# Optimization experiments

Hardware: AMD Instinct MI355X
Metric: run time of the kernel (lower is better)

## Reference

```python
import jax, jax.numpy as jnp
from jax import lax
import numpy as np

R = 4            # correlation displacement radius -> 81 channels
BACKWARP = 1.25  # fltBackwarp for intLevel=4


def leaky(x):
    return jnp.where(x >= 0, x, 0.1 * x)


def conv2d(x, w, b):
    # 3x3, stride 1, pad 1, NCHW/OIHW
    y = lax.conv_general_dilated(x, w, (1, 1), ((1, 1), (1, 1)),
                                 dimension_numbers=('NCHW', 'OIHW', 'NCHW'))
    return y + b[None, :, None, None]


def conv_transpose2d(x, w, b):
    # PyTorch ConvTranspose2d(k=4, s=2, p=1); w is (Cin, Cout, 4, 4)
    wt = jnp.transpose(jnp.flip(w, (2, 3)), (1, 0, 2, 3))  # -> OIHW
    y = lax.conv_general_dilated(x, wt, (1, 1), ((2, 2), (2, 2)),
                                 lhs_dilation=(2, 2),
                                 dimension_numbers=('NCHW', 'OIHW', 'NCHW'))
    return y + b[None, :, None, None]


def correlation(f1, f2):
    # cost volume: mean over channels of f1 * shifted f2, zero padding, 81 taps
    B, C, H, W = f1.shape
    f2p = jnp.pad(f2, ((0, 0), (0, 0), (R, R), (R, R)))
    outs = [jnp.mean(f1 * lax.dynamic_slice(f2p, (0, 0, dy, dx), (B, C, H, W)), axis=1)
            for dy in range(2 * R + 1) for dx in range(2 * R + 1)]
    return jnp.stack(outs, axis=1)  # (B, 81, H, W)


def flow_warp(feat, flow):
    # bilinear grid_sample, padding_mode='zeros', align_corners=True
    # align_corners=True normalization round-trips, so sample at pixel coords
    B, C, H, W = feat.shape
    ys, xs = jnp.meshgrid(jnp.arange(H, dtype=flow.dtype),
                          jnp.arange(W, dtype=flow.dtype), indexing='ij')
    px = xs[None] + flow[:, 0]  # (B,H,W)
    py = ys[None] + flow[:, 1]
    x0 = jnp.floor(px); y0 = jnp.floor(py)
    wx = px - x0; wy = py - y0
    featl = jnp.transpose(feat, (0, 2, 3, 1))  # (B,H,W,C)
    bidx = jnp.arange(B)[:, None, None]

    def gather(yi, xi):
        valid = (yi >= 0) & (yi < H) & (xi >= 0) & (xi < W)
        yc = jnp.clip(yi, 0, H - 1).astype(jnp.int32)
        xc = jnp.clip(xi, 0, W - 1).astype(jnp.int32)
        return featl[bidx, yc, xc] * valid[..., None].astype(feat.dtype)

    out = (gather(y0, x0) * ((1 - wy) * (1 - wx))[..., None]
           + gather(y0, x0 + 1) * ((1 - wy) * wx)[..., None]
           + gather(y0 + 1, x0) * (wy * (1 - wx))[..., None]
           + gather(y0 + 1, x0 + 1) * (wy * wx)[..., None])
    return jnp.transpose(out, (0, 3, 1, 2))


def setup_inputs() -> dict:
    key = jax.random.key(0)
    ks = jax.random.split(key, 24)
    B, C, H, W = 8, 96, 64, 128
    intCurrent = 81 + 96 + 2 + 2          # 181
    prevC = (81 + 128 + 2 + 2) + 128 + 128 + 96 + 64 + 32  # 661
    s = 0.05
    inp = {
        'tenOne': jax.random.normal(ks[0], (B, C, H, W), jnp.float32),
        'tenTwo': jax.random.normal(ks[1], (B, C, H, W), jnp.float32),
        'prev_flow': jax.random.normal(ks[2], (B, 2, H // 2, W // 2), jnp.float32),
        'prev_feat': jax.random.normal(ks[3], (B, prevC, H // 2, W // 2), jnp.float32),
        'w_upflow': jax.random.normal(ks[4], (2, 2, 4, 4), jnp.float32) * s,
        'b_upflow': jax.random.normal(ks[5], (2,), jnp.float32) * s,
        'w_upfeat': jax.random.normal(ks[6], (prevC, 2, 4, 4), jnp.float32) * s,
        'b_upfeat': jax.random.normal(ks[7], (2,), jnp.float32) * s,
    }
    c = intCurrent
    dims = [(128, c), (128, c + 128), (96, c + 256), (64, c + 352), (32, c + 416), (2, c + 448)]
    for i, (co, ci) in enumerate(dims):
        inp[f'w{i+1}'] = jax.random.normal(ks[8 + 2 * i], (co, ci, 3, 3), jnp.float32) * s
        inp[f'b{i+1}'] = jax.random.normal(ks[9 + 2 * i], (co,), jnp.float32) * s
    return inp


def reference(tenOne, tenTwo, prev_flow, prev_feat,
              w_upflow, b_upflow, w_upfeat, b_upfeat,
              w1, b1, w2, b2, w3, b3, w4, b4, w5, b5, w6, b6):
    tenFlow = conv_transpose2d(prev_flow, w_upflow, b_upflow)   # (B,2,H,W)
    upFeat = conv_transpose2d(prev_feat, w_upfeat, b_upfeat)    # (B,2,H,W)
    warped = flow_warp(tenTwo, tenFlow * BACKWARP)
    vol = leaky(correlation(tenOne, warped))                    # (B,81,H,W)
    feat = jnp.concatenate([vol, tenOne, tenFlow, upFeat], axis=1)  # 181 ch
    feat = jnp.concatenate([leaky(conv2d(feat, w1, b1)), feat], axis=1)
    feat = jnp.concatenate([leaky(conv2d(feat, w2, b2)), feat], axis=1)
    feat = jnp.concatenate([leaky(conv2d(feat, w3, b3)), feat], axis=1)
    feat = jnp.concatenate([leaky(conv2d(feat, w4, b4)), feat], axis=1)
    feat = jnp.concatenate([leaky(conv2d(feat, w5, b5)), feat], axis=1)
    flow = leaky(conv2d(feat, w6, b6))                          # netSix is a ConvBlock
    return flow, feat
```

## Files before the change

kernel.cpp:

```cpp
#include <hip/hip_runtime.h>

#define W 128
#define H 64
#define HW 8192
#define NB 8
#define NPIX 65536
#define CHSZ 2097152L

typedef __attribute__((ext_vector_type(8))) short short8;
typedef __attribute__((ext_vector_type(4))) float floatx4;

__device__ __forceinline__ float leakyf(float v) { return v >= 0.f ? v : 0.1f * v; }

__device__ __forceinline__ unsigned short f2bf(float f) {
    unsigned u = __float_as_uint(f);
    u += 0x7FFF + ((u >> 16) & 1);
    return (unsigned short)(u >> 16);
}
__device__ __forceinline__ float bf2f(unsigned short s) {
    return __uint_as_float((unsigned)s << 16);
}


__global__ void upconv2_kernel(const float* __restrict__ in, int Cin, int Hin, int Win,
                               const float* __restrict__ w, const float* __restrict__ bias,
                               float* __restrict__ out, long obs)
{
    const int x = threadIdx.x;
    const int y = blockIdx.x;
    const int b = blockIdx.y;

    const int p = (y + 1) & 1;
    const int kyA = p, kyB = p + 2;
    const int iyA = (y + 1 - kyA) >> 1;
    const int iyB = (y + 1 - kyB) >> 1;
    const bool vyA = (iyA >= 0) && (iyA < Hin);
    const bool vyB = (iyB >= 0) && (iyB < Hin);

    const int q = (x + 1) & 1;
    const int kxA = q, kxB = q + 2;
    const int ixA = (x + 1 - kxA) >> 1;
    const int ixB = (x + 1 - kxB) >> 1;
    const bool vxA = (ixA >= 0) && (ixA < Win);
    const bool vxB = (ixB >= 0) && (ixB < Win);

    const bool mAA = vyA && vxA, mAB = vyA && vxB, mBA = vyB && vxA, mBB = vyB && vxB;
    const int oAA = iyA * Win + ixA, oAB = iyA * Win + ixB;
    const int oBA = iyB * Win + ixA, oBB = iyB * Win + ixB;
    const int wAA = kyA * 4 + kxA, wAB = kyA * 4 + kxB;
    const int wBA = kyB * 4 + kxA, wBB = kyB * 4 + kxB;

    float acc0 = bias[0];
    float acc1 = bias[1];
    const long hwin = (long)Hin * Win;
    const float* ip = in + (long)b * Cin * hwin;
    const float* wp = w;
    for (int ci = 0; ci < Cin; ++ci, ip += hwin, wp += 32) {
        float vAA = mAA ? ip[oAA] : 0.f;
        float vAB = mAB ? ip[oAB] : 0.f;
        float vBA = mBA ? ip[oBA] : 0.f;
        float vBB = mBB ? ip[oBB] : 0.f;
        acc0 += vAA * wp[wAA] + vAB * wp[wAB] + vBA * wp[wBA] + vBB * wp[wBB];
        acc1 += vAA * wp[16 + wAA] + vAB * wp[16 + wAB] + vBA * wp[16 + wBA] + vBB * wp[16 + wBB];
    }
    long o = (long)b * obs + y * W + x;
    out[o]      = acc0;
    out[o + HW] = acc1;
}

__global__ __launch_bounds__(1024) void upconv2_split_kernel(
    const float* __restrict__ in, int Cin, int Hin, int Win,
    const float* __restrict__ w, const float* __restrict__ bias,
    float* __restrict__ out, long obs)
{
    __shared__ float red[8][128][2];

    const int x = threadIdx.x & 127;
    const int s = threadIdx.x >> 7;
    const int y = blockIdx.x;
    const int b = blockIdx.y;

    const int p = (y + 1) & 1;
    const int kyA = p, kyB = p + 2;
    const int iyA = (y + 1 - kyA) >> 1;
    const int iyB = (y + 1 - kyB) >> 1;
    const bool vyA = (iyA >= 0) && (iyA < Hin);
    const bool vyB = (iyB >= 0) && (iyB < Hin);

    const int q = (x + 1) & 1;
    const int kxA = q, kxB = q + 2;
    const int ixA = (x + 1 - kxA) >> 1;
    const int ixB = (x + 1 - kxB) >> 1;
    const bool vxA = (ixA >= 0) && (ixA < Win);
    const bool vxB = (ixB >= 0) && (ixB < Win);

    const bool mAA = vyA && vxA, mAB = vyA && vxB, mBA = vyB && vxA, mBB = vyB && vxB;
    const int oAA = iyA * Win + ixA, oAB = iyA * Win + ixB;
    const int oBA = iyB * Win + ixA, oBB = iyB * Win + ixB;
    const int wAA = kyA * 4 + kxA, wAB = kyA * 4 + kxB;
    const int wBA = kyB * 4 + kxA, wBB = kyB * 4 + kxB;

    const int per = (Cin + 7) / 8;
    const int lo = s * per;
    const int hi = min(lo + per, Cin);

    float acc0 = 0.f, acc1 = 0.f;
    const long hwin = (long)Hin * Win;
    const float* ip = in + (long)b * Cin * hwin + (long)lo * hwin;
    const float* wp = w + lo * 32;
    for (int ci = lo; ci < hi; ++ci, ip += hwin, wp += 32) {
        float vAA = mAA ? ip[oAA] : 0.f;
        float vAB = mAB ? ip[oAB] : 0.f;
        float vBA = mBA ? ip[oBA] : 0.f;
        float vBB = mBB ? ip[oBB] : 0.f;
        acc0 += vAA * wp[wAA] + vAB * wp[wAB] + vBA * wp[wBA] + vBB * wp[wBB];
        acc1 += vAA * wp[16 + wAA] + vAB * wp[16 + wAB] + vBA * wp[16 + wBA] + vBB * wp[16 + wBB];
    }
    red[s][x][0] = acc0;
    red[s][x][1] = acc1;
    __syncthreads();
    if (s == 0) {
        float a0 = bias[0], a1 = bias[1];
        #pragma unroll
        for (int t = 0; t < 8; ++t) { a0 += red[t][x][0]; a1 += red[t][x][1]; }
        long o = (long)b * obs + y * W + x;
        out[o]      = a0;
        out[o + HW] = a1;
    }
}

__global__ __launch_bounds__(512) void warp_nhwc_kernel(
    const float* __restrict__ tenTwo, const float* __restrict__ flow4,
    unsigned short* __restrict__ warped_n)
{
    __shared__ unsigned short tile[128 * 98];

    const int x   = threadIdx.x & 127;
    const int sub = threadIdx.x >> 7;
    const int row = blockIdx.x;
    const int b = row >> 6;
    const int y = row & 63;

    const long fb = (long)b * 2 * HW + y * W + x;
    const float px = (float)x + 1.25f * flow4[fb];
    const float py = (float)y + 1.25f * flow4[fb + HW];

    const float x0f = floorf(px), y0f = floorf(py);
    const float wx = px - x0f, wy = py - y0f;
    const int x0 = (int)x0f, y0 = (int)y0f;
    const int x1 = x0 + 1,   y1 = y0 + 1;

    const bool vx0 = (x0 >= 0) && (x0 < W), vx1 = (x1 >= 0) && (x1 < W);
    const bool vy0 = (y0 >= 0) && (y0 < H), vy1 = (y1 >= 0) && (y1 < H);
    const int cx0 = min(max(x0, 0), W - 1), cx1 = min(max(x1, 0), W - 1);
    const int cy0 = min(max(y0, 0), H - 1), cy1 = min(max(y1, 0), H - 1);

    const float w00 = (1.f - wy) * (1.f - wx) * ((vy0 && vx0) ? 1.f : 0.f);
    const float w01 = (1.f - wy) * wx         * ((vy0 && vx1) ? 1.f : 0.f);
    const float w10 = wy * (1.f - wx)         * ((vy1 && vx0) ? 1.f : 0.f);
    const float w11 = wy * wx                 * ((vy1 && vx1) ? 1.f : 0.f);

    const int o00 = cy0 * W + cx0, o01 = cy0 * W + cx1;
    const int o10 = cy1 * W + cx0, o11 = cy1 * W + cx1;

    for (int i = 0; i < 24; ++i) {
        const int c = sub * 24 + i;
        const float* pch = tenTwo + (long)(b * 96 + c) * HW;
        const float v = pch[o00] * w00 + pch[o01] * w01 + pch[o10] * w10 + pch[o11] * w11;
        tile[x * 98 + c] = f2bf(v);
    }
    __syncthreads();

    unsigned short* op = warped_n + (long)row * 128 * 96;
    for (int u = threadIdx.x; u < 1536; u += 512) {
        const int pxi = u / 12;
        const int cc = u - pxi * 12;
        const unsigned short* tp = tile + pxi * 98 + cc * 8;
        uint4 v;
        v.x = *(const unsigned*)(tp + 0);
        v.y = *(const unsigned*)(tp + 2);
        v.z = *(const unsigned*)(tp + 4);
        v.w = *(const unsigned*)(tp + 6);
        *(uint4*)(op + u * 8) = v;
    }
}

__global__ __launch_bounds__(512) void corr_kernel(
    const float* __restrict__ tenOne, const unsigned short* __restrict__ warped_n,
    unsigned short* __restrict__ featn)
{
    const int x  = threadIdx.x & 127;
    const int kg = threadIdx.x >> 7;
    const int row = blockIdx.x;
    const int b = row >> 6;
    const int y = row & 63;
    const long pix = (long)row * W + x;

    float one[96];
    const float* op = tenOne + (long)b * 96 * HW + y * W + x;
    #pragma unroll
    for (int j = 0; j < 96; ++j) one[j] = op[(long)j * HW];

    const int k0 = kg * 21;
    const int k1 = min(k0 + 21, 81);
    for (int k = k0; k < k1; ++k) {
        const int dy = k / 9 - 4, dx = k % 9 - 4;
        const int yy = y + dy, xx = x + dx;
        float acc = 0.f;
        if (yy >= 0 && yy < H && xx >= 0 && xx < W) {
            const unsigned short* wp = warped_n + ((long)(b * H + yy) * W + xx) * 96;
            #pragma unroll
            for (int c4 = 0; c4 < 12; ++c4) {
                const uint4 v = *(const uint4*)(wp + c4 * 8);
                unsigned uu[4] = {v.x, v.y, v.z, v.w};
                #pragma unroll
                for (int e = 0; e < 4; ++e) {
                    const float flo = __uint_as_float(uu[e] << 16);
                    const float fhi = __uint_as_float(uu[e] & 0xffff0000u);
                    acc += one[c4 * 8 + e * 2] * flo + one[c4 * 8 + e * 2 + 1] * fhi;
                }
            }
        }
        const int c = 448 + k;
        featn[((long)(c >> 5) * NPIX + pix) * 32 + (c & 31)] = f2bf(leakyf(acc * (1.f / 96.f)));
    }
}

__global__ void pack_kernel(const float* __restrict__ one, const float* __restrict__ flow4,
                            const float* __restrict__ up4, unsigned short* __restrict__ featn)
{
    const long t = (long)blockIdx.x * 256 + threadIdx.x;
    const long b = t >> 13;
    const long p = t & (HW - 1);
    unsigned short buf[8];
    for (int cc = 0; cc < 14; ++cc) {
        const int cbase = 528 + cc * 8;
        #pragma unroll
        for (int j = 0; j < 8; ++j) {
            const int c = cbase + j;
            float v;
            if (c < 529)      v = 0.f;
            else if (c < 625) v = one[(b * 96 + (c - 529)) * HW + p];
            else if (c < 627) v = flow4[(b * 2 + (c - 625)) * HW + p];
            else if (c < 629) v = up4[(b * 2 + (c - 627)) * HW + p];
            else              v = 0.f;
            buf[j] = f2bf(v);
        }
        *(uint4*)(featn + ((long)(cbase >> 5) * NPIX + t) * 32 + (cbase & 31)) = *(const uint4*)buf;
    }
}

__global__ void unpack_kernel(const unsigned short* __restrict__ featn, float* __restrict__ out)
{
    const long t = (long)blockIdx.x * 256 + threadIdx.x;
    const long b = t >> 13;
    const long p = t & (HW - 1);
    const unsigned short* f = featn + t * 32;
    float* ob = out + b * 629L * HW + p;
    for (int cc = 0; cc < 20; ++cc) {
        const unsigned short* fc = f + (long)cc * CHSZ;
        #pragma unroll
        for (int g = 0; g < 4; ++g) {
            uint4 v = *(const uint4*)(fc + g * 8);
            unsigned short s[8];
            *(uint4*)s = v;
            #pragma unroll
            for (int j = 0; j < 8; ++j) {
                const int c = cc * 32 + g * 8 + j;
                if (c < 629) ob[(long)c * HW] = bf2f(s[j]);
            }
        }
    }
}

__global__ void wcvt_kernel(const float* __restrict__ w, unsigned short* __restrict__ wt,
                            int Cout, int Cin, int NFC, long total)
{
    const long t = (long)blockIdx.x * 256 + threadIdx.x;
    if (t >= total) return;
    const int j    = (int)(t & 7);
    const int lane = (int)((t >> 3) & 63);
    long r = t >> 9;
    const int nf  = (int)(r % NFC);  r /= NFC;
    const int tap = (int)(r % 9);
    const int kc  = (int)(r / 9);
    const int l15 = lane & 15, q = lane >> 4;
    const int co = nf * 16 + l15;
    const int ci = kc * 32 + q * 8 + j;
    float v = 0.f;
    if (co < Cout && ci < Cin) v = w[((long)co * Cin + ci) * 9 + tap];
    wt[t] = f2bf(v);
}

template<int NFT>
__global__ __launch_bounds__(512, 4) void conv_mfma(
    const unsigned short* __restrict__ featn, int c0, int nchunks,
    const unsigned short* __restrict__ wt, const float* __restrict__ bias,
    unsigned short* __restrict__ outf, int oc0, float* __restrict__ flowout)
{
    constexpr int NFW = (NFT + 1) / 2;
    __shared__ unsigned short tile[2][3 * 130 * 40];

    const int row = blockIdx.x;
    const int b = row >> 6;
    const int y = row & 63;
    const int tid = threadIdx.x;
    const int lane = tid & 63;
    const int wave = tid >> 6;
    const int mg = wave & 3;
    const int nh = wave >> 2;
    const int l15 = lane & 15;
    const int q = lane >> 4;
    const bool active = (nh * NFW) < NFT;

    int gofs[4];
    int lofs[4];
    #pragma unroll
    for (int it = 0; it < 4; ++it) {
        const int u = tid + it * 512;
        const int pr = u >> 2;
        const int sub = u & 3;
        const int r = (pr >= 260) ? 2 : (pr >= 130 ? 1 : 0);
        const int xx = pr - r * 130;
        const int gy = y + r - 1, gx = xx - 1;
        const bool inu = (u < 1560);
        const bool inb = inu && (gy >= 0) && (gy < H) && (gx >= 0) && (gx < W);
        gofs[it] = inb ? (((b * H + gy) * W + gx) * 32 + sub * 8) : -1;
        lofs[it] = inu ? (pr * 40 + sub * 8) : -1;
    }

    floatx4 acc[2][NFW];
    #pragma unroll
    for (int mf = 0; mf < 2; ++mf)
        #pragma unroll
        for (int nf = 0; nf < NFW; ++nf)
            acc[mf][nf] = (floatx4){0.f, 0.f, 0.f, 0.f};

    const unsigned short* fb = featn + (long)(c0 >> 5) * CHSZ;
    const unsigned short* wlane = wt + lane * 8;

    uint4 rg[4];
    #pragma unroll
    for (int it = 0; it < 4; ++it)
        rg[it] = (gofs[it] >= 0) ? *(const uint4*)(fb + gofs[it]) : make_uint4(0u, 0u, 0u, 0u);
    #pragma unroll
    for (int it = 0; it < 4; ++it)
        if (lofs[it] >= 0) *(uint4*)&tile[0][lofs[it]] = rg[it];
    if (nchunks > 1) {
        const unsigned short* fn = fb + CHSZ;
        #pragma unroll
        for (int it = 0; it < 4; ++it)
            rg[it] = (gofs[it] >= 0) ? *(const uint4*)(fn + gofs[it]) : make_uint4(0u, 0u, 0u, 0u);
    }
    __syncthreads();

    for (int kc = 0; kc < nchunks; ++kc) {
        const int cur = kc & 1;

        if (kc + 1 < nchunks) {
            #pragma unroll
            for (int it = 0; it < 4; ++it)
                if (lofs[it] >= 0) *(uint4*)&tile[cur ^ 1][lofs[it]] = rg[it];
        }
        if (kc + 2 < nchunks) {
            const unsigned short* fn = fb + (long)(kc + 2) * CHSZ;
            #pragma unroll
            for (int it = 0; it < 4; ++it)
                rg[it] = (gofs[it] >= 0) ? *(const uint4*)(fn + gofs[it]) : make_uint4(0u, 0u, 0u, 0u);
        }

        if (active) {
            #pragma unroll
            for (int ky = 0; ky < 3; ++ky) {
                #pragma unroll
                for (int kx = 0; kx < 3; ++kx) {
                    const int tap = ky * 3 + kx;
                    const short8 a0 = *(const short8*)&tile[cur][(ky * 130 + mg * 32 + l15 + kx) * 40 + q * 8];
                    const short8 a1 = *(const short8*)&tile[cur][(ky * 130 + mg * 32 + 16 + l15 + kx) * 40 + q * 8];
                    const unsigned short* wb = wlane + ((long)((kc * 9 + tap) * NFT + nh * NFW) << 9);
                    #pragma unroll
                    for (int nf = 0; nf < NFW; ++nf) {
                        const short8 bf = *(const short8*)(wb + ((long)nf << 9));
                        acc[0][nf] = __builtin_amdgcn_mfma_f32_16x16x32_bf16(a0, bf, acc[0][nf], 0, 0, 0);
                        acc[1][nf] = __builtin_amdgcn_mfma_f32_16x16x32_bf16(a1, bf, acc[1][nf], 0, 0, 0);
                    }
                }
            }
        }
        __syncthreads();
    }

    if (flowout == nullptr) {
        if (active) {
            float bv[NFW];
            #pragma unroll
            for (int nf = 0; nf < NFW; ++nf) bv[nf] = bias[(nh * NFW + nf) * 16 + l15];
            const int cchunk0 = oc0 >> 5;
            #pragma unroll
            for (int mf = 0; mf < 2; ++mf) {
                const int xb = mg * 32 + mf * 16 + q * 4;
                #pragma unroll
                for (int r = 0; r < 4; ++r) {
                    const long pixo = (long)row * W + xb + r;
                    #pragma unroll
                    for (int nf = 0; nf < NFW; ++nf) {
                        const int nfg = nh * NFW + nf;
                        float v = acc[mf][nf][r] + bv[nf];
                        const long a = ((long)(cchunk0 + (nfg >> 1)) * NPIX + pixo) * 32 + (nfg & 1) * 16 + l15;
                        outf[a] = f2bf(leakyf(v));
                    }
                }
            }
        }
    } else {
        if (active && l15 < 2) {
            const float bb = bias[l15];
            #pragma unroll
            for (int mf = 0; mf < 2; ++mf) {
                const int xb = mg * 32 + mf * 16 + q * 4;
                #pragma unroll
                for (int r = 0; r < 4; ++r) {
                    float v = acc[mf][0][r] + bb;
                    flowout[((long)b * 2 + l15) * HW + y * W + xb + r] = leakyf(v);
                }
            }
        }
    }
}

extern "C" void kernel_launch(void* const* d_in, const int* in_sizes, int n_in,
                              void* d_out, int out_size, void* d_ws, size_t ws_size,
                              hipStream_t stream)
{
    const float* tenOne    = (const float*)d_in[0];
    const float* tenTwo    = (const float*)d_in[1];
    const float* prev_flow = (const float*)d_in[2];
    const float* prev_feat = (const float*)d_in[3];
    const float* w_upflow  = (const float*)d_in[4];
    const float* b_upflow  = (const float*)d_in[5];
    const float* w_upfeat  = (const float*)d_in[6];
    const float* b_upfeat  = (const float*)d_in[7];
    const float* wc[6] = {(const float*)d_in[8],  (const float*)d_in[10], (const float*)d_in[12],
                          (const float*)d_in[14], (const float*)d_in[16], (const float*)d_in[18]};
    const float* bc[6] = {(const float*)d_in[9],  (const float*)d_in[11], (const float*)d_in[13],
                          (const float*)d_in[15], (const float*)d_in[17], (const float*)d_in[19]};

    float* flow_out = (float*)d_out;
    float* feat_out = flow_out + (long)NB * 2 * HW;

    char* ws = (char*)d_ws;
    unsigned short* featn    = (unsigned short*)ws;
    unsigned short* warped_n = (unsigned short*)ws;
    float* flow4 = (float*)(ws + 83886080L);
    float* up4   = (float*)(ws + 84410368L);
    unsigned short* wt1 = (unsigned short*)(ws + 84934656L);
    unsigned short* wt2 = (unsigned short*)(ws + 85377024L);
    unsigned short* wt3 = (unsigned short*)(ws + 86114304L);
    unsigned short* wt4 = (unsigned short*)(ws + 86888448L);
    unsigned short* wt5 = (unsigned short*)(ws + 87515136L);
    unsigned short* wt6 = (unsigned short*)(ws + 87865344L);
    unsigned short* wts[6] = {wt1, wt2, wt3, wt4, wt5, wt6};

    const int Cout[6] = {128, 128, 96, 64, 32, 2};
    const int Cin [6] = {181, 309, 437, 533, 597, 629};
    const int NCH [6] = {6, 10, 14, 17, 19, 20};
    const int NFC [6] = {8, 8, 6, 4, 2, 1};
    const int c0  [6] = {448, 320, 192, 96, 32, 0};
    const int oc0 [6] = {320, 192, 96, 32, 0, 0};

    for (int i = 0; i < 6; ++i) {
        long total = (long)NCH[i] * 9 * NFC[i] * 512;
        wcvt_kernel<<<(int)((total + 255) / 256), 256, 0, stream>>>(
            wc[i], wts[i], Cout[i], Cin[i], NFC[i], total);
    }

    upconv2_kernel<<<dim3(H, NB), W, 0, stream>>>(prev_flow, 2, 32, 64,
                                                  w_upflow, b_upflow, flow4, (long)(2 * HW));
    upconv2_split_kernel<<<dim3(H, NB), 1024, 0, stream>>>(prev_feat, 661, 32, 64,
                                                           w_upfeat, b_upfeat, up4, (long)(2 * HW));

    pack_kernel<<<256, 256, 0, stream>>>(tenOne, flow4, up4, featn);
    warp_nhwc_kernel<<<512, 512, 0, stream>>>(tenTwo, flow4, warped_n);
    corr_kernel<<<512, 512, 0, stream>>>(tenOne, warped_n, featn);

    conv_mfma<8><<<512, 512, 0, stream>>>(featn, c0[0], NCH[0], wts[0], bc[0], featn, oc0[0], nullptr);
    conv_mfma<8><<<512, 512, 0, stream>>>(featn, c0[1], NCH[1], wts[1], bc[1], featn, oc0[1], nullptr);
    conv_mfma<6><<<512, 512, 0, stream>>>(featn, c0[2], NCH[2], wts[2], bc[2], featn, oc0[2], nullptr);
    conv_mfma<4><<<512, 512, 0, stream>>>(featn, c0[3], NCH[3], wts[3], bc[3], featn, oc0[3], nullptr);
    conv_mfma<2><<<512, 512, 0, stream>>>(featn, c0[4], NCH[4], wts[4], bc[4], featn, oc0[4], nullptr);
    conv_mfma<1><<<512, 512, 0, stream>>>(featn, c0[5], NCH[5], wts[5], bc[5], featn, 0, flow_out);

    unpack_kernel<<<256, 256, 0, stream>>>(featn, feat_out);
}
```

Baseline: 901.6 us.

## Stage warped features in shared memory for correlation and coalesce featn writes

The warp kernel now writes warped features in a channel-group-blocked layout (16 channels per group). The correlation kernel loops over 6 channel groups, loading a 9-row halo tile of warped features into shared memory once per block instead of every thread reading 96 channels per displacement from global memory. Results are transposed through shared memory so featn channel blocks are written with coalesced 16-byte stores. The first 15 tenOne channels are folded into the same block output, so the pack kernel skips them. This adds barriers and about 39 KB of LDS per block, which may reduce occupancy.

Result: faster. 784.0 us (-13.0%).

```diff
diff --git a/kernel.cpp b/kernel.cpp
--- a/kernel.cpp
+++ b/kernel.cpp
@@ -171,7 +171,7 @@
     }
     __syncthreads();
 
-    unsigned short* op = warped_n + (long)row * 128 * 96;
+    const long pixbase = (long)row * 128;
     for (int u = threadIdx.x; u < 1536; u += 512) {
         const int pxi = u / 12;
         const int cc = u - pxi * 12;
@@ -181,7 +181,7 @@
         v.y = *(const unsigned*)(tp + 2);
         v.z = *(const unsigned*)(tp + 4);
         v.w = *(const unsigned*)(tp + 6);
-        *(uint4*)(op + u * 8) = v;
+        *(uint4*)(warped_n + ((long)(cc >> 1) * NPIX + pixbase + pxi) * 16 + (cc & 1) * 8) = v;
     }
 }
 
@@ -189,40 +189,88 @@
     const float* __restrict__ tenOne, const unsigned short* __restrict__ warped_n,
     unsigned short* __restrict__ featn)
 {
-    const int x  = threadIdx.x & 127;
-    const int kg = threadIdx.x >> 7;
+    __shared__ unsigned short smem[19584];
+
+    const int tid = threadIdx.x;
+    const int x  = tid & 127;
+    const int kg = tid >> 7;
     const int row = blockIdx.x;
     const int b = row >> 6;
     const int y = row & 63;
-    const long pix = (long)row * W + x;
-
-    float one[96];
-    const float* op = tenOne + (long)b * 96 * HW + y * W + x;
-    #pragma unroll
-    for (int j = 0; j < 96; ++j) one[j] = op[(long)j * HW];
+
+    float acc[21];
+    #pragma unroll
+    for (int i = 0; i < 21; ++i) acc[i] = 0.f;
 
     const int k0 = kg * 21;
-    const int k1 = min(k0 + 21, 81);
-    for (int k = k0; k < k1; ++k) {
-        const int dy = k / 9 - 4, dx = k % 9 - 4;
-        const int yy = y + dy, xx = x + dx;
-        float acc = 0.f;
-        if (yy >= 0 && yy < H && xx >= 0 && xx < W) {
-            const unsigned short* wp = warped_n + ((long)(b * H + yy) * W + xx) * 96;
-            #pragma unroll
-            for (int c4 = 0; c4 < 12; ++c4) {
-                const uint4 v = *(const uint4*)(wp + c4 * 8);
-                unsigned uu[4] = {v.x, v.y, v.z, v.w};
-                #pragma unroll
-                for (int e = 0; e < 4; ++e) {
-                    const float flo = __uint_as_float(uu[e] << 16);
-                    const float fhi = __uint_as_float(uu[e] & 0xffff0000u);
-                    acc += one[c4 * 8 + e * 2] * flo + one[c4 * 8 + e * 2 + 1] * fhi;
-                }
+
+    for (int cg = 0; cg < 6; ++cg) {
+        float one_c[16];
+        const float* op = tenOne + ((long)b * 96 + cg * 16) * HW + y * W + x;
+        #pragma unroll
+        for (int j = 0; j < 16; ++j) one_c[j] = op[(long)j * HW];
+
+        if (cg) __syncthreads();
+        for (int u = tid; u < 2448; u += 512) {
+            const int sub = u & 1;
+            const int pr = u >> 1;
+            const int r = pr / 136;
+            const int xx = pr - r * 136;
+            const int gy = y + r - 4, gx = xx - 4;
+            uint4 v = make_uint4(0u, 0u, 0u, 0u);
+            if (gy >= 0 && gy < H && gx >= 0 && gx < W)
+                v = *(const uint4*)(warped_n + ((long)cg * NPIX + (b * H + gy) * W + gx) * 16 + sub * 8);
+            *(uint4*)&smem[((sub * 9 + r) * 136 + xx) * 8] = v;
+        }
+        __syncthreads();
+
+        #pragma unroll
+        for (int i = 0; i < 21; ++i) {
+            const int k = min(k0 + i, 80);
+            const int ry = k / 9;
+            const int rx = x + (k - ry * 9);
+            const uint4 va = *(const uint4*)&smem[(ry * 136 + rx) * 8];
+            const uint4 vb = *(const uint4*)&smem[((9 + ry) * 136 + rx) * 8];
+            const unsigned ua[4] = {va.x, va.y, va.z, va.w};
+            const unsigned ub[4] = {vb.x, vb.y, vb.z, vb.w};
+            float s = 0.f;
+            #pragma unroll
+            for (int e = 0; e < 4; ++e) {
+                s += one_c[2 * e]     * __uint_as_float(ua[e] << 16)
+                   + one_c[2 * e + 1] * __uint_as_float(ua[e] & 0xffff0000u)
+                   + one_c[8 + 2 * e]     * __uint_as_float(ub[e] << 16)
+                   + one_c[8 + 2 * e + 1] * __uint_as_float(ub[e] & 0xffff0000u);
             }
-        }
-        const int c = 448 + k;
-        featn[((long)(c >> 5) * NPIX + pix) * 32 + (c & 31)] = f2bf(leakyf(acc * (1.f / 96.f)));
+            acc[i] += s;
+        }
+    }
+
+    __syncthreads();
+
+    #pragma unroll
+    for (int i = 0; i < 21; ++i) {
+        const int k = k0 + i;
+        if (k <= 80) smem[k * 132 + x] = f2bf(leakyf(acc[i] * (1.f / 96.f)));
+    }
+    if (kg == 0) {
+        const float* op0 = tenOne + (long)b * 96 * HW + y * W + x;
+        #pragma unroll
+        for (int j = 0; j < 15; ++j)
+            smem[(81 + j) * 132 + x] = f2bf(op0[(long)j * HW]);
+    }
+    __syncthreads();
+
+    #pragma unroll
+    for (int it = 0; it < 3; ++it) {
+        const int u = tid + it * 512;
+        const int sub = u & 3;
+        const int px = (u >> 2) & 127;
+        const int cc = u >> 9;
+        const int t0 = cc * 32 + sub * 8;
+        unsigned short bufo[8];
+        #pragma unroll
+        for (int j = 0; j < 8; ++j) bufo[j] = smem[(t0 + j) * 132 + px];
+        *(uint4*)(featn + ((long)(14 + cc) * NPIX + (long)row * 128 + px) * 32 + sub * 8) = *(const uint4*)bufo;
     }
 }
 
@@ -233,14 +281,13 @@
     const long b = t >> 13;
     const long p = t & (HW - 1);
     unsigned short buf[8];
-    for (int cc = 0; cc < 14; ++cc) {
-        const int cbase = 528 + cc * 8;
+    for (int cc = 0; cc < 12; ++cc) {
+        const int cbase = 544 + cc * 8;
         #pragma unroll
         for (int j = 0; j < 8; ++j) {
             const int c = cbase + j;
             float v;
-            if (c < 529)      v = 0.f;
-            else if (c < 625) v = one[(b * 96 + (c - 529)) * HW + p];
+            if (c < 625)      v = one[(b * 96 + (c - 529)) * HW + p];
             else if (c < 627) v = flow4[(b * 2 + (c - 625)) * HW + p];
             else if (c < 629) v = up4[(b * 2 + (c - 627)) * HW + p];
             else              v = 0.f;
```
